# Kernel optimization log

Measured on AMD Instinct MI355X. Metric: run time of the kernel, lower is better.

The kernel has to match this reference:

```python
import jax, jax.numpy as jnp
import numpy as np

NUM_EMBEDDINGS = 1024
EMBEDDING_DIM = 64
DECAY = 0.99
EPS = 1e-5


def setup_inputs() -> dict:
    key = jax.random.key(0)
    k0, k1, k2 = jax.random.split(key, 3)
    return {
        "inputs": jax.random.normal(k0, (32, 64, 64, EMBEDDING_DIM), dtype=jnp.float32),
        "embeddings": jax.random.normal(k1, (NUM_EMBEDDINGS, EMBEDDING_DIM), dtype=jnp.float32),
        "ema_cluster_size": jnp.ones((NUM_EMBEDDINGS,), dtype=jnp.float32),
        "ema_w": jax.random.normal(k2, (NUM_EMBEDDINGS, EMBEDDING_DIM), dtype=jnp.float32),
    }


def reference(inputs, embeddings, ema_cluster_size, ema_w):
    input_shape = inputs.shape
    flat = inputs.reshape(-1, EMBEDDING_DIM)  # [N, D]

    input_sq = jnp.sum(flat * flat, axis=1, keepdims=True)          # [N, 1]
    codebook_sq = jnp.sum(embeddings * embeddings, axis=1)          # [K]
    dot = jnp.matmul(flat, embeddings.T)                            # [N, K]
    distances = input_sq + codebook_sq - 2.0 * dot

    encoding_indices = jnp.argmin(distances, axis=-1)               # [N]
    encodings = jax.nn.one_hot(encoding_indices, NUM_EMBEDDINGS, dtype=flat.dtype)  # [N, K]
    quantized_flat = jnp.take(embeddings, encoding_indices, axis=0)  # [N, D]

    # --- EMA updates (training path) ---
    current_counts = jax.ops.segment_sum(
        jnp.ones_like(encoding_indices, dtype=flat.dtype),
        encoding_indices, num_segments=NUM_EMBEDDINGS)              # == sum(encodings, 0)
    upd_cluster = ema_cluster_size * DECAY + (1.0 - DECAY) * current_counts
    n = jnp.sum(upd_cluster)
    upd_cluster = (upd_cluster + EPS) / (n + NUM_EMBEDDINGS * EPS) * n

    # sum of inputs assigned to each code == encodings.T @ flat
    assignment_sums = jax.ops.segment_sum(flat, encoding_indices,
                                          num_segments=NUM_EMBEDDINGS)  # [K, D]
    upd_ema_w = ema_w * DECAY + (1.0 - DECAY) * assignment_sums
    upd_embeddings = upd_ema_w / (upd_cluster[:, None] + EPS)

    quantization_loss = jnp.mean((flat - quantized_flat) ** 2).reshape((1,))
    quantized = quantized_flat.reshape(input_shape)
    quantized_flow = inputs + jax.lax.stop_gradient(quantized - inputs)

    usage_counts = current_counts
    usage_ratio = jnp.sum((usage_counts > 0).astype(jnp.float32)) / NUM_EMBEDDINGS

    return (quantized_flow, encodings, usage_ratio, quantization_loss,
            upd_embeddings, upd_cluster, upd_ema_w)
```

## Files before the change

kernel.cpp:

```cpp
#include <hip/hip_runtime.h>
#include <hip/hip_bf16.h>

#define NK 1024
#define ND 64
#define NV 131072
#define BR 128
#define DECAY_F 0.99f
#define OMD_F 0.01f
#define EPS_F 1e-5f
#define KEPS_F 0.01024f

typedef const __attribute__((address_space(1))) void* gas1_t;
typedef __attribute__((address_space(3))) void* las3_t;
#define GLOAD_LDS16(gp, lp) \
    __builtin_amdgcn_global_load_lds((gas1_t)(gp), (las3_t)(lp), 16, 0, 0)
#define MEMFENCE asm volatile("" ::: "memory")


__global__ __launch_bounds__(256) void vq_prep(const float* __restrict__ emb,
                                               float* __restrict__ csq,
                                               int* __restrict__ cnt,
                                               double* loss,
                                               float4* __restrict__ acc4)
{
    int k = blockIdx.x * 256 + threadIdx.x;
    cnt[k] = 0;
    if (k == 0) *loss = 0.0;
    float4 z = make_float4(0.f, 0.f, 0.f, 0.f);
#pragma unroll
    for (int i = 0; i < 16; ++i) acc4[k + i * 1024] = z;
    float p[ND];
    const float4* e4 = reinterpret_cast<const float4*>(emb + (size_t)k * ND);
#pragma unroll
    for (int i = 0; i < 16; ++i) {
        float4 v = e4[i];
        p[4*i+0] = __fmul_rn(v.x, v.x);
        p[4*i+1] = __fmul_rn(v.y, v.y);
        p[4*i+2] = __fmul_rn(v.z, v.z);
        p[4*i+3] = __fmul_rn(v.w, v.w);
    }
    float r[8];
#pragma unroll
    for (int j = 0; j < 8; ++j) r[j] = p[j];
#pragma unroll
    for (int i = 8; i < ND; i += 8)
#pragma unroll
        for (int j = 0; j < 8; ++j) r[j] = __fadd_rn(r[j], p[i+j]);
    csq[k] = __fadd_rn(__fadd_rn(__fadd_rn(r[0], r[1]), __fadd_rn(r[2], r[3])),
                       __fadd_rn(__fadd_rn(r[4], r[5]), __fadd_rn(r[6], r[7])));
}

__global__ __launch_bounds__(256, 2) void vq_assign(
    const float* __restrict__ x_in, const float* __restrict__ emb,
    const float* __restrict__ csq, float* __restrict__ out_qf,
    float* __restrict__ out_enc, float* __restrict__ acc_buf,
    int* __restrict__ cnt, double* __restrict__ loss_acc)
{
    __shared__ __align__(16) float xs[BR * ND];
    __shared__ __align__(16) float es[128 * ND];
    __shared__ float csq_s[NK];
    __shared__ float isq_s[BR];
    __shared__ double lds_ls[4];

    const int tid  = threadIdx.x;
    const int lane = tid & 63;
    const int wv   = tid >> 6;
    const int tx   = tid & 15;
    const int ty   = tid >> 4;
    const int txs  = tx & 7;
    const int tys  = ty & 7;
    const size_t rowbase = (size_t)blockIdx.x * BR;
    const float4 zv = make_float4(0.f, 0.f, 0.f, 0.f);

#pragma unroll
    for (int c = 0; c < 8; ++c) {
        int f = tid + c * 256;
        int row = f >> 4, ch = f & 15;
        int sch = ch ^ (row & 7);
        GLOAD_LDS16(x_in + rowbase * ND + row * ND + sch * 4, &xs[f * 4]);
    }
#pragma unroll
    for (int c = 0; c < 8; ++c) {
        int f = tid + c * 256;
        int row = f >> 4, ch = f & 15;
        int sch = ch ^ (row & 7);
        GLOAD_LDS16(emb + (size_t)row * ND + sch * 4, &es[f * 4]);
    }
#pragma unroll
    for (int c = 0; c < 4; ++c) csq_s[tid + c * 256] = csq[tid + c * 256];
    __syncthreads();

    if (tid < BR) {
        const int rs = tid & 7;
        const float* xr = &xs[tid * ND];
        float r[8];
        {
            float4 a = *(const float4*)&xr[(0 ^ rs) * 4];
            float4 b = *(const float4*)&xr[(1 ^ rs) * 4];
            r[0] = __fmul_rn(a.x, a.x); r[1] = __fmul_rn(a.y, a.y);
            r[2] = __fmul_rn(a.z, a.z); r[3] = __fmul_rn(a.w, a.w);
            r[4] = __fmul_rn(b.x, b.x); r[5] = __fmul_rn(b.y, b.y);
            r[6] = __fmul_rn(b.z, b.z); r[7] = __fmul_rn(b.w, b.w);
        }
#pragma unroll
        for (int g = 1; g < 8; ++g) {
            float4 a = *(const float4*)&xr[((2*g)   ^ rs) * 4];
            float4 b = *(const float4*)&xr[((2*g+1) ^ rs) * 4];
            r[0] = __fadd_rn(r[0], __fmul_rn(a.x, a.x));
            r[1] = __fadd_rn(r[1], __fmul_rn(a.y, a.y));
            r[2] = __fadd_rn(r[2], __fmul_rn(a.z, a.z));
            r[3] = __fadd_rn(r[3], __fmul_rn(a.w, a.w));
            r[4] = __fadd_rn(r[4], __fmul_rn(b.x, b.x));
            r[5] = __fadd_rn(r[5], __fmul_rn(b.y, b.y));
            r[6] = __fadd_rn(r[6], __fmul_rn(b.z, b.z));
            r[7] = __fadd_rn(r[7], __fmul_rn(b.w, b.w));
        }
        isq_s[tid] = __fadd_rn(__fadd_rn(__fadd_rn(r[0], r[1]), __fadd_rn(r[2], r[3])),
                               __fadd_rn(__fadd_rn(r[4], r[5]), __fadd_rn(r[6], r[7])));
    }

    float best[8];
    int   bestk[8];
#pragma unroll
    for (int i = 0; i < 8; ++i) { best[i] = 3.4e38f; bestk[i] = 0; }

    for (int t = 0; t < 8; ++t) {
        float acc[8][8];
#pragma unroll
        for (int i = 0; i < 8; ++i)
#pragma unroll
            for (int j = 0; j < 8; ++j) acc[i][j] = 0.f;

        for (int ch = 0; ch < 16; ++ch) {
            const int xo = (ch ^ tys) * 4;
            const int eo = (ch ^ txs) * 4;
            float4 xf[8], ef[8];
#pragma unroll
            for (int i = 0; i < 8; ++i)
                xf[i] = *(const float4*)&xs[(ty + 16*i) * ND + xo];
#pragma unroll
            for (int j = 0; j < 8; ++j)
                ef[j] = *(const float4*)&es[(tx + 16*j) * ND + eo];
#pragma unroll
            for (int i = 0; i < 8; ++i) {
#pragma unroll
                for (int j = 0; j < 8; ++j) {
                    float a = acc[i][j];
                    a = __builtin_fmaf(xf[i].x, ef[j].x, a);
                    a = __builtin_fmaf(xf[i].y, ef[j].y, a);
                    a = __builtin_fmaf(xf[i].z, ef[j].z, a);
                    a = __builtin_fmaf(xf[i].w, ef[j].w, a);
                    acc[i][j] = a;
                }
            }
        }

#pragma unroll
        for (int i = 0; i < 8; ++i) {
            float isq = isq_s[ty + 16*i];
#pragma unroll
            for (int j = 0; j < 8; ++j) {
                float dist = __fsub_rn(__fadd_rn(isq, csq_s[t * 128 + tx + 16*j]),
                                       __fmul_rn(2.0f, acc[i][j]));
                if (dist < best[i]) { best[i] = dist; bestk[i] = t * 128 + tx + 16*j; }
            }
        }

        MEMFENCE;
        __builtin_amdgcn_s_barrier();
        MEMFENCE;

        if (t < 7) {
#pragma unroll
            for (int c = 0; c < 8; ++c) {
                int f = tid + c * 256;
                int row = f >> 4, ch = f & 15;
                int sch = ch ^ (row & 7);
                GLOAD_LDS16(emb + (size_t)(t + 1) * 128 * ND + row * ND + sch * 4,
                            &es[f * 4]);
            }
        }
        MEMFENCE;
        {
            float4* encb = reinterpret_cast<float4*>(out_enc + (rowbase + t * 16) * NK);
#pragma unroll
            for (int i = 0; i < 16; ++i)
                encb[tid + i * 256] = zv;
        }
        if (t < 7) {
            asm volatile("s_waitcnt vmcnt(16)" ::: "memory");
        }
        MEMFENCE;
        __builtin_amdgcn_s_barrier();
        MEMFENCE;
    }

    float* red_d = es;
    int*   red_i = reinterpret_cast<int*>(es + 2048);
#pragma unroll
    for (int i = 0; i < 8; ++i) {
        red_d[(ty + 16*i) * 16 + tx] = best[i];
        red_i[(ty + 16*i) * 16 + tx] = bestk[i];
    }
    asm volatile("s_waitcnt lgkmcnt(0)" ::: "memory");
    __builtin_amdgcn_s_barrier();
    MEMFENCE;
    if (tid < BR) {
        float bd = red_d[tid * 16];
        int   bk = red_i[tid * 16];
#pragma unroll
        for (int c = 1; c < 16; ++c) {
            float d  = red_d[tid * 16 + c];
            int   k2 = red_i[tid * 16 + c];
            if (d < bd || (d == bd && k2 < bk)) { bd = d; bk = k2; }
        }
        atomicAdd(&cnt[bk], 1);
        red_i[tid * 16] = bk;
    }
    asm volatile("s_waitcnt lgkmcnt(0)" ::: "memory");
    __builtin_amdgcn_s_barrier();
    MEMFENCE;

    float lsum = 0.f;
    const int lsw = (lane >> 2);
    for (int r = 0; r < 32; ++r) {
        int rl = wv * 32 + r;
        int kr = red_i[rl * 16];
        size_t grow = rowbase + rl;
        float xv = xs[rl * ND + ((lsw ^ (rl & 7)) << 2) + (lane & 3)];
        float ev = emb[(size_t)kr * ND + lane];
        out_qf[grow * ND + lane] = __fadd_rn(xv, __fsub_rn(ev, xv));
        float dd = __fsub_rn(xv, ev);
        lsum = __builtin_fmaf(dd, dd, lsum);
        atomicAdd(&acc_buf[(size_t)kr * ND + lane], xv);
    }
    double ls = (double)lsum;
#pragma unroll
    for (int off = 32; off >= 1; off >>= 1) ls += __shfl_xor(ls, off, 64);
    if (lane == 0) lds_ls[wv] = ls;

    asm volatile("s_waitcnt vmcnt(0)" ::: "memory");
    __syncthreads();

    if (tid < BR) {
        int bk = red_i[tid * 16];
        out_enc[(rowbase + tid) * NK + bk] = 1.0f;
    }
    if (tid == 0)
        atomicAdd(loss_acc, (lds_ls[0] + lds_ls[1]) + (lds_ls[2] + lds_ls[3]));
}

__global__ __launch_bounds__(256) void vq_scan(
    const int* __restrict__ cnt, const float* __restrict__ ema_cs,
    const double* __restrict__ loss_acc, float* __restrict__ ucf_ws,
    float* __restrict__ out_uc, float* __restrict__ out_usage,
    float* __restrict__ out_loss)
{
    __shared__ float uc_s[1024];
    __shared__ int   usage_s;
    __shared__ float n_s;
    const int tid  = threadIdx.x;
    if (tid == 0) usage_s = 0;
    __syncthreads();

    int ucount = 0;
#pragma unroll
    for (int j = 0; j < 4; ++j) {
        int k = tid * 4 + j;
        int c = cnt[k];
        if (c > 0) ucount++;
        uc_s[k] = __fadd_rn(__fmul_rn(ema_cs[k], DECAY_F), __fmul_rn(OMD_F, (float)c));
    }
    atomicAdd(&usage_s, ucount);
    __syncthreads();

    if (tid < 64) {
        int b = tid >> 3, j = tid & 7;
        float r = uc_s[b * 128 + j];
#pragma unroll
        for (int i = 1; i < 16; ++i)
            r = __fadd_rn(r, uc_s[b * 128 + 8 * i + j]);
        r = __fadd_rn(r, __shfl_xor(r, 1, 64));
        r = __fadd_rn(r, __shfl_xor(r, 2, 64));
        r = __fadd_rn(r, __shfl_xor(r, 4, 64));
        r = __fadd_rn(r, __shfl_xor(r, 8, 64));
        r = __fadd_rn(r, __shfl_xor(r, 16, 64));
        r = __fadd_rn(r, __shfl_xor(r, 32, 64));
        if (tid == 0) {
            n_s = r;
            *out_usage = __fdiv_rn((float)usage_s, 1024.0f);
            *out_loss  = (float)(*loss_acc / 8388608.0);
        }
    }
    __syncthreads();

    const float n = n_s;
#pragma unroll
    for (int j = 0; j < 4; ++j) {
        int k = tid * 4 + j;
        float ucfv = __fmul_rn(__fdiv_rn(__fadd_rn(uc_s[k], EPS_F), __fadd_rn(n, KEPS_F)), n);
        out_uc[k] = ucfv;
        ucf_ws[k] = ucfv;
    }
}

__global__ __launch_bounds__(256) void vq_final(
    const float* __restrict__ acc_buf, const float* __restrict__ ema_w,
    const float* __restrict__ ucf, float* __restrict__ out_updw,
    float* __restrict__ out_upde)
{
    int gid = blockIdx.x * 256 + threadIdx.x;
    int k = gid >> 6;
    float w = __fadd_rn(__fmul_rn(ema_w[gid], DECAY_F), __fmul_rn(OMD_F, acc_buf[gid]));
    out_updw[gid] = w;
    out_upde[gid] = __fdiv_rn(w, __fadd_rn(ucf[k], EPS_F));
}

extern "C" void kernel_launch(void* const* d_in, const int* in_sizes, int n_in,
                              void* d_out, int out_size, void* d_ws, size_t ws_size,
                              hipStream_t stream)
{
    const float* x_in   = (const float*)d_in[0];
    const float* emb    = (const float*)d_in[1];
    const float* ema_cs = (const float*)d_in[2];
    const float* ema_w  = (const float*)d_in[3];

    float* out_qf    = (float*)d_out;
    float* out_enc   = out_qf + (size_t)NV * ND;
    float* out_usage = out_enc + (size_t)NV * NK;
    float* out_loss  = out_usage + 1;
    float* out_upde  = out_loss + 1;
    float* out_uc    = out_upde + (size_t)NK * ND;
    float* out_updw  = out_uc + NK;

    char* ws = (char*)d_ws;
    float*  ws_csq    = (float*)(ws);
    int*    ws_cnt    = (int*)(ws + 4096);
    float*  ws_ucf    = (float*)(ws + 16384);
    double* ws_loss   = (double*)(ws + 20480);
    float*  ws_acc    = (float*)(ws + 1597440);

    vq_prep<<<4, 256, 0, stream>>>(emb, ws_csq, ws_cnt, ws_loss, (float4*)ws_acc);
    vq_assign<<<NV / BR, 256, 0, stream>>>(x_in, emb, ws_csq, out_qf, out_enc,
                                           ws_acc, ws_cnt, ws_loss);
    vq_scan<<<1, 256, 0, stream>>>(ws_cnt, ema_cs, ws_loss, ws_ucf,
                                   out_uc, out_usage, out_loss);
    vq_final<<<256, 256, 0, stream>>>(ws_acc, ema_w, ws_ucf, out_updw, out_upde);
}
```

Baseline: 300.2 us.

## Read codebook directly from global memory instead of staging through LDS

```diff
diff --git a/kernel.cpp b/kernel.cpp
--- a/kernel.cpp
+++ b/kernel.cpp
@@ -50,16 +50,17 @@
                        __fadd_rn(__fadd_rn(r[4], r[5]), __fadd_rn(r[6], r[7])));
 }
 
-__global__ __launch_bounds__(256, 2) void vq_assign(
+__global__ __launch_bounds__(256, 3) void vq_assign(
     const float* __restrict__ x_in, const float* __restrict__ emb,
     const float* __restrict__ csq, float* __restrict__ out_qf,
     float* __restrict__ out_enc, float* __restrict__ acc_buf,
     int* __restrict__ cnt, double* __restrict__ loss_acc)
 {
     __shared__ __align__(16) float xs[BR * ND];
-    __shared__ __align__(16) float es[128 * ND];
     __shared__ float csq_s[NK];
     __shared__ float isq_s[BR];
+    __shared__ float red_d[BR * 16];
+    __shared__ int   red_i[BR * 16];
     __shared__ double lds_ls[4];
 
     const int tid  = threadIdx.x;
@@ -67,7 +68,6 @@
     const int wv   = tid >> 6;
     const int tx   = tid & 15;
     const int ty   = tid >> 4;
-    const int txs  = tx & 7;
     const int tys  = ty & 7;
     const size_t rowbase = (size_t)blockIdx.x * BR;
     const float4 zv = make_float4(0.f, 0.f, 0.f, 0.f);
@@ -78,13 +78,6 @@
         int row = f >> 4, ch = f & 15;
         int sch = ch ^ (row & 7);
         GLOAD_LDS16(x_in + rowbase * ND + row * ND + sch * 4, &xs[f * 4]);
-    }
-#pragma unroll
-    for (int c = 0; c < 8; ++c) {
-        int f = tid + c * 256;
-        int row = f >> 4, ch = f & 15;
-        int sch = ch ^ (row & 7);
-        GLOAD_LDS16(emb + (size_t)row * ND + sch * 4, &es[f * 4]);
     }
 #pragma unroll
     for (int c = 0; c < 4; ++c) csq_s[tid + c * 256] = csq[tid + c * 256];
@@ -118,6 +111,7 @@
         isq_s[tid] = __fadd_rn(__fadd_rn(__fadd_rn(r[0], r[1]), __fadd_rn(r[2], r[3])),
                                __fadd_rn(__fadd_rn(r[4], r[5]), __fadd_rn(r[6], r[7])));
     }
+    __syncthreads();
 
     float best[8];
     int   bestk[8];
@@ -125,6 +119,7 @@
     for (int i = 0; i < 8; ++i) { best[i] = 3.4e38f; bestk[i] = 0; }
 
     for (int t = 0; t < 8; ++t) {
+        const float* et = emb + (size_t)(t * 128 + tx) * ND;
         float acc[8][8];
 #pragma unroll
         for (int i = 0; i < 8; ++i)
@@ -133,14 +128,13 @@
 
         for (int ch = 0; ch < 16; ++ch) {
             const int xo = (ch ^ tys) * 4;
-            const int eo = (ch ^ txs) * 4;
             float4 xf[8], ef[8];
+#pragma unroll
+            for (int j = 0; j < 8; ++j)
+                ef[j] = *(const float4*)(et + j * (16 * ND) + ch * 4);
 #pragma unroll
             for (int i = 0; i < 8; ++i)
                 xf[i] = *(const float4*)&xs[(ty + 16*i) * ND + xo];
-#pragma unroll
-            for (int j = 0; j < 8; ++j)
-                ef[j] = *(const float4*)&es[(tx + 16*j) * ND + eo];
 #pragma unroll
             for (int i = 0; i < 8; ++i) {
 #pragma unroll
@@ -166,37 +160,14 @@
             }
         }
 
-        MEMFENCE;
-        __builtin_amdgcn_s_barrier();
-        MEMFENCE;
-
-        if (t < 7) {
-#pragma unroll
-            for (int c = 0; c < 8; ++c) {
-                int f = tid + c * 256;
-                int row = f >> 4, ch = f & 15;
-                int sch = ch ^ (row & 7);
-                GLOAD_LDS16(emb + (size_t)(t + 1) * 128 * ND + row * ND + sch * 4,
-                            &es[f * 4]);
-            }
-        }
-        MEMFENCE;
         {
             float4* encb = reinterpret_cast<float4*>(out_enc + (rowbase + t * 16) * NK);
 #pragma unroll
             for (int i = 0; i < 16; ++i)
                 encb[tid + i * 256] = zv;
         }
-        if (t < 7) {
-            asm volatile("s_waitcnt vmcnt(16)" ::: "memory");
-        }
-        MEMFENCE;
-        __builtin_amdgcn_s_barrier();
-        MEMFENCE;
-    }
-
-    float* red_d = es;
-    int*   red_i = reinterpret_cast<int*>(es + 2048);
+    }
+
 #pragma unroll
     for (int i = 0; i < 8; ++i) {
         red_d[(ty + 16*i) * 16 + tx] = best[i];
```

After: 628.7 us. 2.09x slower.
